# Kernel optimization log

Hardware: AMD Instinct MI355X
Metric: run time of the kernel (lower is better)

## Reference

```python
import jax, jax.numpy as jnp
import numpy as np

N = 10000      # nodes
E = 160000     # edges (before self-loops)
G = 64         # graphs in batch
IN_DIM = 6
HID = 128
H1 = 4         # heads in gat1
OUT_DIM = 4
NEG_SLOPE = 0.2  # PyG GATConv default


def setup_inputs() -> dict:
    key = jax.random.key(0)
    ks = jax.random.split(key, 16)
    s = 0.1
    return {
        "x": jax.random.normal(ks[0], (N, IN_DIM), dtype=jnp.float32),
        "edge_index": jax.random.randint(ks[1], (2, E), 0, N, dtype=jnp.int64),
        "batch": jnp.sort(jax.random.randint(ks[2], (N,), 0, G, dtype=jnp.int64)),
        # gat1: 4 heads, concat
        "W1": jax.random.normal(ks[3], (IN_DIM, H1 * HID), dtype=jnp.float32) * s,
        "a_src1": jax.random.normal(ks[4], (H1, HID), dtype=jnp.float32) * s,
        "a_dst1": jax.random.normal(ks[5], (H1, HID), dtype=jnp.float32) * s,
        "b1": jnp.zeros((H1 * HID,), dtype=jnp.float32),
        # gat2: 1 head, mean (concat=False)
        "W2": jax.random.normal(ks[6], (H1 * HID, HID), dtype=jnp.float32) * s,
        "a_src2": jax.random.normal(ks[7], (1, HID), dtype=jnp.float32) * s,
        "a_dst2": jax.random.normal(ks[8], (1, HID), dtype=jnp.float32) * s,
        "b2": jnp.zeros((HID,), dtype=jnp.float32),
        # MLP head
        "mw1": jax.random.normal(ks[9], (HID, HID), dtype=jnp.float32) * s,
        "mb1": jnp.zeros((HID,), dtype=jnp.float32),
        "mw2": jax.random.normal(ks[10], (HID, OUT_DIM), dtype=jnp.float32) * s,
        "mb2": jnp.zeros((OUT_DIM,), dtype=jnp.float32),
    }


def _gat_conv(x, src, dst, W, a_src, a_dst, b, concat):
    # x: [N, F_in]; src/dst: [E'] (self-loops already included)
    n = x.shape[0]
    H, C = a_src.shape
    xl = (x @ W).reshape(n, H, C)               # [N, H, C]
    es = jnp.sum(xl * a_src, axis=-1)           # [N, H]
    ed = jnp.sum(xl * a_dst, axis=-1)           # [N, H]
    e = jax.nn.leaky_relu(es[src] + ed[dst], NEG_SLOPE)   # [E', H]
    # segment softmax over incoming edges of each target node
    m = jax.lax.stop_gradient(jax.ops.segment_max(e, dst, num_segments=n))
    ex = jnp.exp(e - m[dst])
    denom = jax.ops.segment_sum(ex, dst, num_segments=n)  # [N, H]
    alpha = ex / denom[dst]
    out = jax.ops.segment_sum(alpha[:, :, None] * xl[src], dst, num_segments=n)  # [N, H, C]
    out = out.reshape(n, H * C) if concat else jnp.mean(out, axis=1)
    return out + b


def _global_mean_pool(x, batch, num_graphs):
    sums = jax.ops.segment_sum(x, batch, num_segments=num_graphs)
    cnt = jax.ops.segment_sum(jnp.ones((x.shape[0],), x.dtype), batch, num_segments=num_graphs)
    return sums / jnp.maximum(cnt, 1.0)[:, None]


def reference(x, edge_index, batch, W1, a_src1, a_dst1, b1, W2, a_src2, a_dst2, b2, mw1, mb1, mw2, mb2):
    n = x.shape[0]
    loops = jnp.arange(n, dtype=edge_index.dtype)
    src = jnp.concatenate([edge_index[0], loops])
    dst = jnp.concatenate([edge_index[1], loops])
    h = jax.nn.relu(_gat_conv(x, src, dst, W1, a_src1, a_dst1, b1, concat=True))
    h = jax.nn.relu(_gat_conv(h, src, dst, W2, a_src2, a_dst2, b2, concat=False))
    g = _global_mean_pool(h, batch, G)
    return jax.nn.relu(g @ mw1 + mb1) @ mw2 + mb2
```

## Files before the change

### kernel.cpp

```cpp
#include <hip/hip_runtime.h>
#include <hip/hip_fp16.h>

#define NEG_SLOPE 0.2f

typedef _Float16 f16x8 __attribute__((ext_vector_type(8)));
typedef float f32x4 __attribute__((ext_vector_type(4)));

__device__ __forceinline__ void edge_sd(const int* ei, int E, int e, int& s, int& d) {
    if (e < E) { s = ei[e]; d = ei[E + e]; }
    else       { int v = e - E; s = v; d = v; }
}

__global__ void zero_kernel(int* p, int n) {
    int i = blockIdx.x * blockDim.x + threadIdx.x;
    if (i < n) p[i] = 0;
}

__global__ void deg_kernel(const int* ei, int E, int N, int* deg) {
    int e = blockIdx.x * blockDim.x + threadIdx.x;
    if (e >= E + N) return;
    int s, d; edge_sd(ei, E, e, s, d);
    atomicAdd(&deg[d], 1);
}

__global__ void scan_kernel(const int* deg, int* offsets, int n) {
    __shared__ int part[1024];
    int t = threadIdx.x;
    int chunk = (n + 1023) / 1024;
    int beg = t * chunk;
    int s = 0;
    for (int i = 0; i < chunk; ++i) {
        int idx = beg + i;
        if (idx < n) s += deg[idx];
    }
    part[t] = s;
    __syncthreads();
    for (int off = 1; off < 1024; off <<= 1) {
        int v = (t >= off) ? part[t - off] : 0;
        __syncthreads();
        part[t] += v;
        __syncthreads();
    }
    if (t == 1023) offsets[n] = part[1023];
    int run = (t == 0) ? 0 : part[t - 1];
    for (int i = 0; i < chunk; ++i) {
        int idx = beg + i;
        if (idx < n) { offsets[idx] = run; run += deg[idx]; }
    }
}

__global__ void fill_kernel(const int* ei, int E, int N, const int* offsets,
                            int* cursor, int* csr_src) {
    int e = blockIdx.x * blockDim.x + threadIdx.x;
    if (e >= E + N) return;
    int s, d; edge_sd(ei, E, e, s, d);
    int pos = offsets[d] + atomicAdd(&cursor[d], 1);
    csr_src[pos] = s;
}

__global__ void w2cvt_kernel(const float* __restrict__ W2, __half* __restrict__ W2t) {
    int i = blockIdx.x * 256 + threadIdx.x;
    int c = i >> 9, k = i & 511;
    W2t[i] = __float2half_rn(W2[k * 128 + c]);
}

__global__ void xw1_attn(const float* __restrict__ x, const float* __restrict__ W1,
                         const float* __restrict__ a_src, const float* __restrict__ a_dst,
                         __half2* __restrict__ xlh, float* __restrict__ es, float* __restrict__ ed,
                         int n) {
    int node = blockIdx.x;
    int t = threadIdx.x;
    __shared__ float xs[6];
    if (t < 6) xs[t] = x[node * 6 + t];
    __syncthreads();
    int j0 = 2 * t, j1 = 2 * t + 1;
    float v0 = 0.f, v1 = 0.f;
#pragma unroll
    for (int k = 0; k < 6; ++k) {
        v0 += xs[k] * W1[k * 512 + j0];
        v1 += xs[k] * W1[k * 512 + j1];
    }
    xlh[(size_t)node * 256 + t] = __floats2half2_rn(v0, v1);
    float ps = v0 * a_src[j0] + v1 * a_src[j1];
    float pd = v0 * a_dst[j0] + v1 * a_dst[j1];
#pragma unroll
    for (int off = 32; off; off >>= 1) {
        ps += __shfl_xor(ps, off);
        pd += __shfl_xor(pd, off);
    }
    int h = t >> 6, lane = t & 63;
    if (lane == 0) { es[node * 4 + h] = ps; ed[node * 4 + h] = pd; }
}

template <int H>
__global__ void alpha_kernel(const float* __restrict__ es, const float* __restrict__ ed,
                             const int* __restrict__ offsets, const int* __restrict__ csr_src,
                             float* __restrict__ alpha, float* __restrict__ dinv, int n) {
    int wave = threadIdx.x >> 6, lane = threadIdx.x & 63;
    int node = blockIdx.x * 4 + wave;
    if (node >= n) return;
    int beg = offsets[node], end = offsets[node + 1];
    float edv[H];
#pragma unroll
    for (int h = 0; h < H; ++h) edv[h] = ed[node * H + h];
    float sum[H];
#pragma unroll
    for (int h = 0; h < H; ++h) sum[h] = 0.f;
    for (int chunk = beg; chunk < end; chunk += 64) {
        int i = chunk + lane;
        bool valid = i < end;
        int s = valid ? csr_src[i] : 0;
        if (H == 4) {
            float4 e4 = valid ? *(const float4*)(es + (size_t)s * 4)
                              : make_float4(0.f, 0.f, 0.f, 0.f);
            float ev[4] = {e4.x, e4.y, e4.z, e4.w};
            float a[4];
#pragma unroll
            for (int h = 0; h < 4; ++h) {
                float w = ev[h] + edv[h];
                w = (w > 0.f) ? w : NEG_SLOPE * w;
                a[h] = valid ? __expf(w) : 0.f;
                sum[h] += a[h];
            }
            if (valid)
                *(float4*)(alpha + (size_t)i * 4) = make_float4(a[0], a[1], a[2], a[3]);
        } else {
            float w = (valid ? es[s] : 0.f) + edv[0];
            w = (w > 0.f) ? w : NEG_SLOPE * w;
            float a = valid ? __expf(w) : 0.f;
            sum[0] += a;
            if (valid) alpha[i] = a;
        }
    }
#pragma unroll
    for (int h = 0; h < H; ++h) {
        float s2 = sum[h];
#pragma unroll
        for (int off = 32; off; off >>= 1) s2 += __shfl_xor(s2, off);
        if (lane == 0) dinv[node * H + h] = 1.f / s2;
    }
}

__global__ void agg4_kernel(const __half* __restrict__ xlh, const float* __restrict__ alpha,
                            const float* __restrict__ dinv, const int* __restrict__ offsets,
                            const int* __restrict__ csr_src, const float* __restrict__ bias,
                            __half* __restrict__ outh, int n) {
    __shared__ int   s_src[4 * 64];
    __shared__ float s_al [4 * 64 * 4];
    int t = threadIdx.x, wave = t >> 6, lane = t & 63;
    int node = blockIdx.x * 4 + wave;
    int beg = offsets[node], end = offsets[node + 1];
    int woff = wave * 64;
    int hsel = lane >> 4;
    float acc[8] = {0.f, 0.f, 0.f, 0.f, 0.f, 0.f, 0.f, 0.f};

    auto accum = [&](float4 r, float a) {
        const __half2* hp = (const __half2*)&r;
        float2 f0 = __half22float2(hp[0]), f1 = __half22float2(hp[1]);
        float2 f2 = __half22float2(hp[2]), f3 = __half22float2(hp[3]);
        acc[0] += a * f0.x; acc[1] += a * f0.y;
        acc[2] += a * f1.x; acc[3] += a * f1.y;
        acc[4] += a * f2.x; acc[5] += a * f2.y;
        acc[6] += a * f3.x; acc[7] += a * f3.y;
    };

    for (int chunk = beg; chunk < end; chunk += 64) {
        int i = chunk + lane;
        bool valid = i < end;
        s_src[woff + lane] = valid ? csr_src[i] : 0;
        float4 av = valid ? *(const float4*)(alpha + (size_t)i * 4)
                          : make_float4(0.f, 0.f, 0.f, 0.f);
        *(float4*)&s_al[(woff + lane) * 4] = av;
        int cnt = end - chunk; if (cnt > 64) cnt = 64;
        int base = 0;
        for (; base + 8 <= cnt; base += 8) {
            int s0 = s_src[woff+base+0], s1 = s_src[woff+base+1];
            int s2 = s_src[woff+base+2], s3 = s_src[woff+base+3];
            int s4 = s_src[woff+base+4], s5 = s_src[woff+base+5];
            int s6 = s_src[woff+base+6], s7 = s_src[woff+base+7];
            float a0 = s_al[(woff+base+0)*4 + hsel], a1 = s_al[(woff+base+1)*4 + hsel];
            float a2 = s_al[(woff+base+2)*4 + hsel], a3 = s_al[(woff+base+3)*4 + hsel];
            float a4 = s_al[(woff+base+4)*4 + hsel], a5 = s_al[(woff+base+5)*4 + hsel];
            float a6 = s_al[(woff+base+6)*4 + hsel], a7 = s_al[(woff+base+7)*4 + hsel];
            float4 r0 = *(const float4*)(xlh + (size_t)s0 * 512 + lane * 8);
            float4 r1 = *(const float4*)(xlh + (size_t)s1 * 512 + lane * 8);
            float4 r2 = *(const float4*)(xlh + (size_t)s2 * 512 + lane * 8);
            float4 r3 = *(const float4*)(xlh + (size_t)s3 * 512 + lane * 8);
            float4 r4 = *(const float4*)(xlh + (size_t)s4 * 512 + lane * 8);
            float4 r5 = *(const float4*)(xlh + (size_t)s5 * 512 + lane * 8);
            float4 r6 = *(const float4*)(xlh + (size_t)s6 * 512 + lane * 8);
            float4 r7 = *(const float4*)(xlh + (size_t)s7 * 512 + lane * 8);
            accum(r0, a0); accum(r1, a1); accum(r2, a2); accum(r3, a3);
            accum(r4, a4); accum(r5, a5); accum(r6, a6); accum(r7, a7);
        }
        for (; base < cnt; ++base) {
            int   sv = s_src[woff + base];
            float av1 = s_al[(woff + base) * 4 + hsel];
            float4 r = *(const float4*)(xlh + (size_t)sv * 512 + lane * 8);
            accum(r, av1);
        }
    }
    float inv = dinv[node * 4 + hsel];
    int c0 = lane * 8;
    float o[8];
#pragma unroll
    for (int k = 0; k < 8; ++k) o[k] = fmaxf(acc[k] * inv + bias[c0 + k], 0.f);
    float4 pack;
    ((__half2*)&pack)[0] = __floats2half2_rn(o[0], o[1]);
    ((__half2*)&pack)[1] = __floats2half2_rn(o[2], o[3]);
    ((__half2*)&pack)[2] = __floats2half2_rn(o[4], o[5]);
    ((__half2*)&pack)[3] = __floats2half2_rn(o[6], o[7]);
    *(float4*)(outh + (size_t)node * 512 + lane * 8) = pack;
}

__global__ void __launch_bounds__(256)
xw2_mfma(const __half* __restrict__ h16, const __half* __restrict__ W2t,
         const float* __restrict__ a_src2, const float* __restrict__ a_dst2,
         __half* __restrict__ xl2h, float* __restrict__ es2, float* __restrict__ ed2, int n) {
    __shared__ float xs[16][132];
    int t = threadIdx.x, w = t >> 6, l = t & 63;
    int m0 = blockIdx.x * 16;
    int rc = l & 15, kg = l >> 4;
    f32x4 acc0 = {0.f, 0.f, 0.f, 0.f}, acc1 = {0.f, 0.f, 0.f, 0.f};
    const __half* arow = h16 + (size_t)(m0 + rc) * 512 + kg * 8;
    const __half* b0p  = W2t + (size_t)(w * 32 + rc) * 512 + kg * 8;
    const __half* b1p  = W2t + (size_t)(w * 32 + 16 + rc) * 512 + kg * 8;
    for (int ks = 0; ks < 512; ks += 32) {
        f16x8 a  = *(const f16x8*)(arow + ks);
        f16x8 b0 = *(const f16x8*)(b0p + ks);
        f16x8 b1 = *(const f16x8*)(b1p + ks);
        acc0 = __builtin_amdgcn_mfma_f32_16x16x32_f16(a, b0, acc0, 0, 0, 0);
        acc1 = __builtin_amdgcn_mfma_f32_16x16x32_f16(a, b1, acc1, 0, 0, 0);
    }
#pragma unroll
    for (int i = 0; i < 4; ++i) {
        xs[kg * 4 + i][w * 32 + rc]      = acc0[i];
        xs[kg * 4 + i][w * 32 + 16 + rc] = acc1[i];
    }
    __syncthreads();
    int r = t >> 4, c0 = (t & 15) * 8;
    float v[8];
#pragma unroll
    for (int j = 0; j < 8; ++j) v[j] = xs[r][c0 + j];
    float4 pack;
    ((__half2*)&pack)[0] = __floats2half2_rn(v[0], v[1]);
    ((__half2*)&pack)[1] = __floats2half2_rn(v[2], v[3]);
    ((__half2*)&pack)[2] = __floats2half2_rn(v[4], v[5]);
    ((__half2*)&pack)[3] = __floats2half2_rn(v[6], v[7]);
    *(float4*)(xl2h + (size_t)(m0 + r) * 128 + c0) = pack;
    float ps = 0.f, pd = 0.f;
#pragma unroll
    for (int j = 0; j < 8; ++j) {
        ps += v[j] * a_src2[c0 + j];
        pd += v[j] * a_dst2[c0 + j];
    }
#pragma unroll
    for (int off = 8; off; off >>= 1) {
        ps += __shfl_xor(ps, off);
        pd += __shfl_xor(pd, off);
    }
    if ((l & 15) == 0) { es2[m0 + r] = ps; ed2[m0 + r] = pd; }
}

__global__ void agg1_kernel(const __half* __restrict__ xlh, const float* __restrict__ alpha,
                            const float* __restrict__ dinv, const int* __restrict__ offsets,
                            const int* __restrict__ csr_src, const float* __restrict__ bias,
                            float* __restrict__ h2, int n) {
    __shared__ int   s_src[4 * 64];
    __shared__ float s_al [4 * 64];
    __shared__ float s_red[4][64][8];
    int t = threadIdx.x, wave = t >> 6, lane = t & 63;
    int node = blockIdx.x * 4 + wave;
    int beg = offsets[node], end = offsets[node + 1];
    int woff = wave * 64;
    int lg = lane >> 4;
    int lc = lane & 15;
    float acc[8] = {0.f, 0.f, 0.f, 0.f, 0.f, 0.f, 0.f, 0.f};

    auto accum = [&](float4 r, float a) {
        const __half2* hp = (const __half2*)&r;
        float2 f0 = __half22float2(hp[0]), f1 = __half22float2(hp[1]);
        float2 f2 = __half22float2(hp[2]), f3 = __half22float2(hp[3]);
        acc[0] += a * f0.x; acc[1] += a * f0.y;
        acc[2] += a * f1.x; acc[3] += a * f1.y;
        acc[4] += a * f2.x; acc[5] += a * f2.y;
        acc[6] += a * f3.x; acc[7] += a * f3.y;
    };

    for (int chunk = beg; chunk < end; chunk += 64) {
        int i = chunk + lane;
        bool valid = i < end;
        s_src[woff + lane] = valid ? csr_src[i] : 0;
        s_al [woff + lane] = valid ? alpha[i] : 0.f;
        int cnt = end - chunk; if (cnt > 64) cnt = 64;
        int base = 0;
        for (; base + 16 <= cnt; base += 16) {
            int e0 = base + lg, e1 = base + 4 + lg, e2 = base + 8 + lg, e3 = base + 12 + lg;
            int   s0 = s_src[woff + e0], s1 = s_src[woff + e1];
            int   s2 = s_src[woff + e2], s3 = s_src[woff + e3];
            float a0 = s_al[woff + e0], a1 = s_al[woff + e1];
            float a2 = s_al[woff + e2], a3 = s_al[woff + e3];
            float4 r0 = *(const float4*)(xlh + (size_t)s0 * 128 + lc * 8);
            float4 r1 = *(const float4*)(xlh + (size_t)s1 * 128 + lc * 8);
            float4 r2 = *(const float4*)(xlh + (size_t)s2 * 128 + lc * 8);
            float4 r3 = *(const float4*)(xlh + (size_t)s3 * 128 + lc * 8);
            accum(r0, a0); accum(r1, a1); accum(r2, a2); accum(r3, a3);
        }
        for (; base < cnt; base += 4) {
            int eg = base + lg;
            bool v = eg < cnt;
            int   sv = v ? s_src[woff + eg] : 0;
            float av = v ? s_al[woff + eg] : 0.f;
            float4 r = *(const float4*)(xlh + (size_t)sv * 128 + lc * 8);
            accum(r, av);
        }
    }
    float4* dst = (float4*)&s_red[wave][lane][0];
    dst[0] = make_float4(acc[0], acc[1], acc[2], acc[3]);
    dst[1] = make_float4(acc[4], acc[5], acc[6], acc[7]);
    int lcs = lane >> 2;
    int pe  = lane & 3;
    float vx = 0.f, vy = 0.f;
#pragma unroll
    for (int g = 0; g < 4; ++g) {
        float2 p = ((float2*)&s_red[wave][g * 16 + lcs][0])[pe];
        vx += p.x; vy += p.y;
    }
    float inv = dinv[node];
    int j0 = 2 * lane;
    float o0 = fmaxf(vx * inv + bias[j0], 0.f);
    float o1 = fmaxf(vy * inv + bias[j0 + 1], 0.f);
    float2* op = (float2*)(h2 + (size_t)node * 128);
    op[lane] = make_float2(o0, o1);
}

__device__ __forceinline__ int lower_bound_i(const int* a, int n, int key) {
    int lo = 0, hi = n;
    while (lo < hi) {
        int mid = (lo + hi) >> 1;
        if (a[mid] < key) lo = mid + 1; else hi = mid;
    }
    return lo;
}

__global__ void __launch_bounds__(512)
pool_mlp_kernel(const float* __restrict__ h2, const int* __restrict__ batch,
                const float* __restrict__ mw1, const float* __restrict__ mb1,
                const float* __restrict__ mw2, const float* __restrict__ mb2,
                float* __restrict__ out, int n) {
    __shared__ float part[4][128];
    __shared__ float gm[128], tbuf[128];
    int g = blockIdx.x, t = threadIdx.x;
    int j = t & 127, rg = t >> 7;
    int a = lower_bound_i(batch, n, g);
    int b = lower_bound_i(batch, n, g + 1);
    float s = 0.f;
    for (int i = a + rg; i < b; i += 4) s += h2[(size_t)i * 128 + j];
    part[rg][j] = s;
    __syncthreads();
    if (t < 128) {
        float cnt = fmaxf((float)(b - a), 1.f);
        gm[j] = (part[0][j] + part[1][j] + part[2][j] + part[3][j]) / cnt;
    }
    __syncthreads();
    if (t < 128) {
        float v = mb1[j];
        for (int k = 0; k < 128; ++k) v += gm[k] * mw1[k * 128 + j];
        tbuf[j] = fmaxf(v, 0.f);
    }
    __syncthreads();
    if (t < 4) {
        float o = mb2[t];
        for (int k = 0; k < 128; ++k) o += tbuf[k] * mw2[k * 4 + t];
        out[g * 4 + t] = o;
    }
}

extern "C" void kernel_launch(void* const* d_in, const int* in_sizes, int n_in,
                              void* d_out, int out_size, void* d_ws, size_t ws_size,
                              hipStream_t stream) {
    const float* x       = (const float*)d_in[0];
    const int*   ei      = (const int*)d_in[1];
    const int*   batch   = (const int*)d_in[2];
    const float* W1      = (const float*)d_in[3];
    const float* a_src1  = (const float*)d_in[4];
    const float* a_dst1  = (const float*)d_in[5];
    const float* b1      = (const float*)d_in[6];
    const float* W2      = (const float*)d_in[7];
    const float* a_src2  = (const float*)d_in[8];
    const float* a_dst2  = (const float*)d_in[9];
    const float* b2      = (const float*)d_in[10];
    const float* mw1     = (const float*)d_in[11];
    const float* mb1     = (const float*)d_in[12];
    const float* mw2     = (const float*)d_in[13];
    const float* mb2     = (const float*)d_in[14];
    float* out = (float*)d_out;

    const int N = in_sizes[0] / 6;
    const int E = in_sizes[1] / 2;
    const int ET = E + N;
    const int G = 64;

    char* ws = (char*)d_ws;
    size_t off = 0;
    auto alloc = [&](size_t bytes) {
        void* p = ws + off;
        off += (bytes + 15) & ~(size_t)15;
        return p;
    };
    __half* xl1h   = (__half*)alloc((size_t)N * 512 * 2);
    __half* hbufh  = (__half*)alloc((size_t)N * 512 * 2);
    __half* xl2h   = (__half*)alloc((size_t)N * 128 * 2);
    float*  h2     = (float*)alloc((size_t)N * 128 * 4);
    __half* W2t    = (__half*)alloc((size_t)512 * 128 * 2);
    float*  es1    = (float*)alloc((size_t)N * 4 * 4);
    float*  ed1    = (float*)alloc((size_t)N * 4 * 4);
    float*  es2    = (float*)alloc((size_t)N * 4);
    float*  ed2    = (float*)alloc((size_t)N * 4);
    float*  dinv1  = (float*)alloc((size_t)N * 4 * 4);
    float*  dinv2  = (float*)alloc((size_t)N * 4);
    float*  alpha1 = (float*)alloc((size_t)ET * 4 * 4);
    float*  alpha2 = (float*)alloc((size_t)ET * 4);
    int*    offsets= (int*)alloc((size_t)(N + 1) * 4);
    int*    zbase  = (int*)alloc((size_t)N * 4 + (size_t)N * 4);
    int*    deg    = zbase;
    int*    cursor = zbase + N;
    int*    csr_src= (int*)alloc((size_t)ET * 4);
    (void)ws_size; (void)n_in; (void)out_size;

    const int zn = 2 * N;

    zero_kernel<<<(zn + 255) / 256, 256, 0, stream>>>(zbase, zn);
    deg_kernel<<<(ET + 255) / 256, 256, 0, stream>>>(ei, E, N, deg);
    w2cvt_kernel<<<(512 * 128) / 256, 256, 0, stream>>>(W2, W2t);
    scan_kernel<<<1, 1024, 0, stream>>>(deg, offsets, N);
    fill_kernel<<<(ET + 255) / 256, 256, 0, stream>>>(ei, E, N, offsets, cursor, csr_src);

    xw1_attn<<<N, 256, 0, stream>>>(x, W1, a_src1, a_dst1, (__half2*)xl1h, es1, ed1, N);
    alpha_kernel<4><<<(N + 3) / 4, 256, 0, stream>>>(es1, ed1, offsets, csr_src, alpha1, dinv1, N);
    agg4_kernel<<<N / 4, 256, 0, stream>>>(xl1h, alpha1, dinv1, offsets, csr_src, b1, hbufh, N);
    xw2_mfma<<<N / 16, 256, 0, stream>>>(hbufh, W2t, a_src2, a_dst2, xl2h, es2, ed2, N);
    alpha_kernel<1><<<(N + 3) / 4, 256, 0, stream>>>(es2, ed2, offsets, csr_src, alpha2, dinv2, N);
    agg1_kernel<<<N / 4, 256, 0, stream>>>(xl2h, alpha2, dinv2, offsets, csr_src, b2, h2, N);
    pool_mlp_kernel<<<G, 512, 0, stream>>>(h2, batch, mw1, mb1, mw2, mb2, out, N);
}
```

Baseline: 209.6 us.

## Fuse attention-weight computation into aggregation kernels and merge setup launches

Removes the separate alpha kernels and computes the exp-scores and softmax denominators inline in both aggregation kernels, so per-edge alpha arrays are no longer written to and read back from memory. Zeroing and the W2 conversion are merged into one setup kernel, and the degree counting is folded into the first projection kernel, which has N blocks of 256 threads and so covers all edges. The net effect is four fewer launches and less global traffic. The cost is extra exp work in the aggregation kernels and a dependence of the edge coverage on the grid size.

```diff
diff --git a/kernel.cpp b/kernel.cpp
--- a/kernel.cpp
+++ b/kernel.cpp
@@ -11,16 +11,15 @@
     else       { int v = e - E; s = v; d = v; }
 }
 
-__global__ void zero_kernel(int* p, int n) {
-    int i = blockIdx.x * blockDim.x + threadIdx.x;
-    if (i < n) p[i] = 0;
-}
-
-__global__ void deg_kernel(const int* ei, int E, int N, int* deg) {
-    int e = blockIdx.x * blockDim.x + threadIdx.x;
-    if (e >= E + N) return;
-    int s, d; edge_sd(ei, E, e, s, d);
-    atomicAdd(&deg[d], 1);
+__global__ void setup_kernel(const float* __restrict__ W2, __half* __restrict__ W2t,
+                             int* __restrict__ zbase, int zn) {
+    int i = blockIdx.x * 256 + threadIdx.x;
+    if (i < 65536) {
+        int c = i >> 9, k = i & 511;
+        W2t[i] = __float2half_rn(W2[k * 128 + c]);
+    } else if (i - 65536 < zn) {
+        zbase[i - 65536] = 0;
+    }
 }
 
 __global__ void scan_kernel(const int* deg, int* offsets, int n) {
@@ -58,16 +57,16 @@
     csr_src[pos] = s;
 }
 
-__global__ void w2cvt_kernel(const float* __restrict__ W2, __half* __restrict__ W2t) {
-    int i = blockIdx.x * 256 + threadIdx.x;
-    int c = i >> 9, k = i & 511;
-    W2t[i] = __float2half_rn(W2[k * 128 + c]);
-}
-
 __global__ void xw1_attn(const float* __restrict__ x, const float* __restrict__ W1,
                          const float* __restrict__ a_src, const float* __restrict__ a_dst,
+                         const int* __restrict__ ei, int E, int ET, int* __restrict__ deg,
                          __half2* __restrict__ xlh, float* __restrict__ es, float* __restrict__ ed,
                          int n) {
+    int ge = blockIdx.x * 256 + threadIdx.x;
+    if (ge < ET) {
+        int s, d; edge_sd(ei, E, ge, s, d);
+        atomicAdd(&deg[d], 1);
+    }
     int node = blockIdx.x;
     int t = threadIdx.x;
     __shared__ float xs[6];
@@ -92,57 +91,8 @@
     if (lane == 0) { es[node * 4 + h] = ps; ed[node * 4 + h] = pd; }
 }
 
-template <int H>
-__global__ void alpha_kernel(const float* __restrict__ es, const float* __restrict__ ed,
-                             const int* __restrict__ offsets, const int* __restrict__ csr_src,
-                             float* __restrict__ alpha, float* __restrict__ dinv, int n) {
-    int wave = threadIdx.x >> 6, lane = threadIdx.x & 63;
-    int node = blockIdx.x * 4 + wave;
-    if (node >= n) return;
-    int beg = offsets[node], end = offsets[node + 1];
-    float edv[H];
-#pragma unroll
-    for (int h = 0; h < H; ++h) edv[h] = ed[node * H + h];
-    float sum[H];
-#pragma unroll
-    for (int h = 0; h < H; ++h) sum[h] = 0.f;
-    for (int chunk = beg; chunk < end; chunk += 64) {
-        int i = chunk + lane;
-        bool valid = i < end;
-        int s = valid ? csr_src[i] : 0;
-        if (H == 4) {
-            float4 e4 = valid ? *(const float4*)(es + (size_t)s * 4)
-                              : make_float4(0.f, 0.f, 0.f, 0.f);
-            float ev[4] = {e4.x, e4.y, e4.z, e4.w};
-            float a[4];
-#pragma unroll
-            for (int h = 0; h < 4; ++h) {
-                float w = ev[h] + edv[h];
-                w = (w > 0.f) ? w : NEG_SLOPE * w;
-                a[h] = valid ? __expf(w) : 0.f;
-                sum[h] += a[h];
-            }
-            if (valid)
-                *(float4*)(alpha + (size_t)i * 4) = make_float4(a[0], a[1], a[2], a[3]);
-        } else {
-            float w = (valid ? es[s] : 0.f) + edv[0];
-            w = (w > 0.f) ? w : NEG_SLOPE * w;
-            float a = valid ? __expf(w) : 0.f;
-            sum[0] += a;
-            if (valid) alpha[i] = a;
-        }
-    }
-#pragma unroll
-    for (int h = 0; h < H; ++h) {
-        float s2 = sum[h];
-#pragma unroll
-        for (int off = 32; off; off >>= 1) s2 += __shfl_xor(s2, off);
-        if (lane == 0) dinv[node * H + h] = 1.f / s2;
-    }
-}
-
-__global__ void agg4_kernel(const __half* __restrict__ xlh, const float* __restrict__ alpha,
-                            const float* __restrict__ dinv, const int* __restrict__ offsets,
+__global__ void agg4_kernel(const __half* __restrict__ xlh, const float* __restrict__ es,
+                            const float* __restrict__ ed, const int* __restrict__ offsets,
                             const int* __restrict__ csr_src, const float* __restrict__ bias,
                             __half* __restrict__ outh, int n) {
     __shared__ int   s_src[4 * 64];
@@ -152,6 +102,8 @@
     int beg = offsets[node], end = offsets[node + 1];
     int woff = wave * 64;
     int hsel = lane >> 4;
+    float4 edv4 = *(const float4*)(ed + (size_t)node * 4);
+    float dn0 = 0.f, dn1 = 0.f, dn2 = 0.f, dn3 = 0.f;
     float acc[8] = {0.f, 0.f, 0.f, 0.f, 0.f, 0.f, 0.f, 0.f};
 
     auto accum = [&](float4 r, float a) {
@@ -167,10 +119,19 @@
     for (int chunk = beg; chunk < end; chunk += 64) {
         int i = chunk + lane;
         bool valid = i < end;
-        s_src[woff + lane] = valid ? csr_src[i] : 0;
-        float4 av = valid ? *(const float4*)(alpha + (size_t)i * 4)
-                          : make_float4(0.f, 0.f, 0.f, 0.f);
-        *(float4*)&s_al[(woff + lane) * 4] = av;
+        int s = valid ? csr_src[i] : 0;
+        s_src[woff + lane] = s;
+        float4 a4 = make_float4(0.f, 0.f, 0.f, 0.f);
+        if (valid) {
+            float4 e4 = *(const float4*)(es + (size_t)s * 4);
+            float wv;
+            wv = e4.x + edv4.x; wv = (wv > 0.f) ? wv : NEG_SLOPE * wv; a4.x = __expf(wv);
+            wv = e4.y + edv4.y; wv = (wv > 0.f) ? wv : NEG_SLOPE * wv; a4.y = __expf(wv);
+            wv = e4.z + edv4.z; wv = (wv > 0.f) ? wv : NEG_SLOPE * wv; a4.z = __expf(wv);
+            wv = e4.w + edv4.w; wv = (wv > 0.f) ? wv : NEG_SLOPE * wv; a4.w = __expf(wv);
+        }
+        *(float4*)&s_al[(woff + lane) * 4] = a4;
+        dn0 += a4.x; dn1 += a4.y; dn2 += a4.z; dn3 += a4.w;
         int cnt = end - chunk; if (cnt > 64) cnt = 64;
         int base = 0;
         for (; base + 8 <= cnt; base += 8) {
@@ -180,7 +141,7 @@
             int s6 = s_src[woff+base+6], s7 = s_src[woff+base+7];
             float a0 = s_al[(woff+base+0)*4 + hsel], a1 = s_al[(woff+base+1)*4 + hsel];
             float a2 = s_al[(woff+base+2)*4 + hsel], a3 = s_al[(woff+base+3)*4 + hsel];
-            float a4 = s_al[(woff+base+4)*4 + hsel], a5 = s_al[(woff+base+5)*4 + hsel];
+            float a4v = s_al[(woff+base+4)*4 + hsel], a5 = s_al[(woff+base+5)*4 + hsel];
             float a6 = s_al[(woff+base+6)*4 + hsel], a7 = s_al[(woff+base+7)*4 + hsel];
             float4 r0 = *(const float4*)(xlh + (size_t)s0 * 512 + lane * 8);
             float4 r1 = *(const float4*)(xlh + (size_t)s1 * 512 + lane * 8);
@@ -191,7 +152,7 @@
             float4 r6 = *(const float4*)(xlh + (size_t)s6 * 512 + lane * 8);
             float4 r7 = *(const float4*)(xlh + (size_t)s7 * 512 + lane * 8);
             accum(r0, a0); accum(r1, a1); accum(r2, a2); accum(r3, a3);
-            accum(r4, a4); accum(r5, a5); accum(r6, a6); accum(r7, a7);
+            accum(r4, a4v); accum(r5, a5); accum(r6, a6); accum(r7, a7);
         }
         for (; base < cnt; ++base) {
             int   sv = s_src[woff + base];
@@ -200,7 +161,15 @@
             accum(r, av1);
         }
     }
-    float inv = dinv[node * 4 + hsel];
+#pragma unroll
+    for (int off = 32; off; off >>= 1) {
+        dn0 += __shfl_xor(dn0, off);
+        dn1 += __shfl_xor(dn1, off);
+        dn2 += __shfl_xor(dn2, off);
+        dn3 += __shfl_xor(dn3, off);
+    }
+    float dsel = (hsel == 0) ? dn0 : (hsel == 1) ? dn1 : (hsel == 2) ? dn2 : dn3;
+    float inv = 1.f / dsel;
     int c0 = lane * 8;
     float o[8];
 #pragma unroll
@@ -262,8 +231,8 @@
     if ((l & 15) == 0) { es2[m0 + r] = ps; ed2[m0 + r] = pd; }
 }
 
-__global__ void agg1_kernel(const __half* __restrict__ xlh, const float* __restrict__ alpha,
-                            const float* __restrict__ dinv, const int* __restrict__ offsets,
+__global__ void agg1_kernel(const __half* __restrict__ xlh, const float* __restrict__ es,
+                            const float* __restrict__ ed, const int* __restrict__ offsets,
                             const int* __restrict__ csr_src, const float* __restrict__ bias,
                             float* __restrict__ h2, int n) {
     __shared__ int   s_src[4 * 64];
@@ -275,6 +244,8 @@
     int woff = wave * 64;
     int lg = lane >> 4;
     int lc = lane & 15;
+    float edv = ed[node];
+    float dn = 0.f;
     float acc[8] = {0.f, 0.f, 0.f, 0.f, 0.f, 0.f, 0.f, 0.f};
 
     auto accum = [&](float4 r, float a) {
@@ -290,8 +261,16 @@
     for (int chunk = beg; chunk < end; chunk += 64) {
         int i = chunk + lane;
         bool valid = i < end;
-        s_src[woff + lane] = valid ? csr_src[i] : 0;
-        s_al [woff + lane] = valid ? alpha[i] : 0.f;
+        int s = valid ? csr_src[i] : 0;
+        s_src[woff + lane] = s;
+        float a = 0.f;
+        if (valid) {
+            float wv = es[s] + edv;
+            wv = (wv > 0.f) ? wv : NEG_SLOPE * wv;
+            a = __expf(wv);
+        }
+        s_al[woff + lane] = a;
+        dn += a;
         int cnt = end - chunk; if (cnt > 64) cnt = 64;
         int base = 0;
         for (; base + 16 <= cnt; base += 16) {
@@ -315,6 +294,8 @@
             accum(r, av);
         }
     }
+#pragma unroll
+    for (int off = 32; off; off >>= 1) dn += __shfl_xor(dn, off);
     float4* dst = (float4*)&s_red[wave][lane][0];
     dst[0] = make_float4(acc[0], acc[1], acc[2], acc[3]);
     dst[1] = make_float4(acc[4], acc[5], acc[6], acc[7]);
@@ -326,7 +307,7 @@
         float2 p = ((float2*)&s_red[wave][g * 16 + lcs][0])[pe];
         vx += p.x; vy += p.y;
     }
-    float inv = dinv[node];
+    float inv = 1.f / dn;
     int j0 = 2 * lane;
     float o0 = fmaxf(vx * inv + bias[j0], 0.f);
     float o1 = fmaxf(vy * inv + bias[j0 + 1], 0.f);
@@ -417,10 +398,6 @@
     float*  ed1    = (float*)alloc((size_t)N * 4 * 4);
     float*  es2    = (float*)alloc((size_t)N * 4);
     float*  ed2    = (float*)alloc((size_t)N * 4);
-    float*  dinv1  = (float*)alloc((size_t)N * 4 * 4);
-    float*  dinv2  = (float*)alloc((size_t)N * 4);
-    float*  alpha1 = (float*)alloc((size_t)ET * 4 * 4);
-    float*  alpha2 = (float*)alloc((size_t)ET * 4);
     int*    offsets= (int*)alloc((size_t)(N + 1) * 4);
     int*    zbase  = (int*)alloc((size_t)N * 4 + (size_t)N * 4);
     int*    deg    = zbase;
@@ -429,18 +406,15 @@
     (void)ws_size; (void)n_in; (void)out_size;
 
     const int zn = 2 * N;
-
-    zero_kernel<<<(zn + 255) / 256, 256, 0, stream>>>(zbase, zn);
-    deg_kernel<<<(ET + 255) / 256, 256, 0, stream>>>(ei, E, N, deg);
-    w2cvt_kernel<<<(512 * 128) / 256, 256, 0, stream>>>(W2, W2t);
+    const int setup_n = 65536 + zn;
+
+    setup_kernel<<<(setup_n + 255) / 256, 256, 0, stream>>>(W2, W2t, zbase, zn);
+    xw1_attn<<<N, 256, 0, stream>>>(x, W1, a_src1, a_dst1, ei, E, ET, deg,
+                                    (__half2*)xl1h, es1, ed1, N);
     scan_kernel<<<1, 1024, 0, stream>>>(deg, offsets, N);
     fill_kernel<<<(ET + 255) / 256, 256, 0, stream>>>(ei, E, N, offsets, cursor, csr_src);
-
-    xw1_attn<<<N, 256, 0, stream>>>(x, W1, a_src1, a_dst1, (__half2*)xl1h, es1, ed1, N);
-    alpha_kernel<4><<<(N + 3) / 4, 256, 0, stream>>>(es1, ed1, offsets, csr_src, alpha1, dinv1, N);
-    agg4_kernel<<<N / 4, 256, 0, stream>>>(xl1h, alpha1, dinv1, offsets, csr_src, b1, hbufh, N);
+    agg4_kernel<<<N / 4, 256, 0, stream>>>(xl1h, es1, ed1, offsets, csr_src, b1, hbufh, N);
     xw2_mfma<<<N / 16, 256, 0, stream>>>(hbufh, W2t, a_src2, a_dst2, xl2h, es2, ed2, N);
-    alpha_kernel<1><<<(N + 3) / 4, 256, 0, stream>>>(es2, ed2, offsets, csr_src, alpha2, dinv2, N);
-    agg1_kernel<<<N / 4, 256, 0, stream>>>(xl2h, alpha2, dinv2, offsets, csr_src, b2, h2, N);
+    agg1_kernel<<<N / 4, 256, 0, stream>>>(xl2h, es2, ed2, offsets, csr_src, b2, h2, N);
     pool_mlp_kernel<<<G, 512, 0, stream>>>(h2, batch, mw1, mb1, mw2, mb2, out, N);
 }
```

Result: faster. 198.7 us (-5.2%).
